# Kernel optimization log

Hardware: AMD Instinct MI355X
Metric: run time of the kernel (lower is better)

The kernel has to match this reference:

```python
import jax, jax.numpy as jnp
import numpy as np

SIGMA = 1.0


def setup_inputs() -> dict:
    key = jax.random.key(0)
    kx, kc = jax.random.split(key)
    B, C, H, W = 8, 64, 64, 64
    NUM_CENTERS = 16
    x = jax.random.normal(kx, (B, C, H, W), dtype=jnp.float32)
    centers = jax.random.normal(kc, (NUM_CENTERS,), dtype=jnp.float32)
    return {"x": x, "centers": centers}


def reference(x, centers):
    # x: (B, C, H, W), centers: (K,)
    B, C, H, W = x.shape
    xr = x.reshape(B, C, H * W, 1)                  # (B, C, HW, 1)
    dist_euc = jnp.abs(xr - centers)                # (B, C, HW, K)
    # soft assignment: softmax over centers of -sigma * |x - c|
    phi_soft = jax.nn.softmax(-SIGMA * dist_euc, axis=-1)
    softout = jnp.sum(phi_soft * centers, axis=-1)  # (B, C, HW)
    # hard assignment: argmax of softmax(-1e7 * |x-c|^2) == nearest center
    idx = jnp.argmin(dist_euc * dist_euc, axis=-1)  # (B, C, HW)
    hardout = centers[idx]                          # (B, C, HW)
    # straight-through: forward = hard, gradient = soft path
    out = jax.lax.stop_gradient(hardout - softout) + softout
    return out.reshape(B, C, H, W)
```

## Files before the change

### kernel.cpp

```cpp
#include <hip/hip_runtime.h>

#define NUM_CENTERS 16

__device__ __forceinline__ float nearest_center(float v, const float* __restrict__ c) {
    float best_val = c[0];
    float best_d   = fabsf(v - c[0]);
#pragma unroll
    for (int i = 1; i < NUM_CENTERS; ++i) {
        float d = fabsf(v - c[i]);
        if (d < best_d) { best_d = d; best_val = c[i]; }
    }
    return best_val;
}

__global__ __launch_bounds__(256) void nearest_center_kernel(
    const float* __restrict__ x,
    const float* __restrict__ centers,
    float* __restrict__ out,
    int n4)
{
    float c[NUM_CENTERS];
#pragma unroll
    for (int i = 0; i < NUM_CENTERS; ++i) c[i] = centers[i];

    int idx = blockIdx.x * blockDim.x + threadIdx.x;
    if (idx < n4) {
        float4 v = reinterpret_cast<const float4*>(x)[idx];
        float4 r;
        r.x = nearest_center(v.x, c);
        r.y = nearest_center(v.y, c);
        r.z = nearest_center(v.z, c);
        r.w = nearest_center(v.w, c);
        reinterpret_cast<float4*>(out)[idx] = r;
    }
}

extern "C" void kernel_launch(void* const* d_in, const int* in_sizes, int n_in,
                              void* d_out, int out_size, void* d_ws, size_t ws_size,
                              hipStream_t stream) {
    const float* x       = (const float*)d_in[0];
    const float* centers = (const float*)d_in[1];
    float* out           = (float*)d_out;

    int n  = in_sizes[0];
    int n4 = n / 4;

    const int block = 256;
    int grid = (n4 + block - 1) / block;
    nearest_center_kernel<<<grid, block, 0, stream>>>(x, centers, out, n4);
}
```

Measured before the change: 62.76 us.

## Use tree-reduction argmin, two float4s per thread, and nontemporal stores

```diff
diff --git a/kernel.cpp b/kernel.cpp
--- a/kernel.cpp
+++ b/kernel.cpp
@@ -2,15 +2,35 @@
 
 #define NUM_CENTERS 16
 
+typedef float nfloat4 __attribute__((ext_vector_type(4)));
+
 __device__ __forceinline__ float nearest_center(float v, const float* __restrict__ c) {
-    float best_val = c[0];
-    float best_d   = fabsf(v - c[0]);
+    float d[NUM_CENTERS];
+    float val[NUM_CENTERS];
 #pragma unroll
-    for (int i = 1; i < NUM_CENTERS; ++i) {
-        float d = fabsf(v - c[i]);
-        if (d < best_d) { best_d = d; best_val = c[i]; }
+    for (int i = 0; i < NUM_CENTERS; ++i) {
+        d[i]   = fabsf(v - c[i]);
+        val[i] = c[i];
     }
-    return best_val;
+#pragma unroll
+    for (int stride = 1; stride < NUM_CENTERS; stride <<= 1) {
+#pragma unroll
+        for (int i = 0; i < NUM_CENTERS; i += 2 * stride) {
+            bool r = d[i + stride] < d[i];
+            d[i]   = r ? d[i + stride]   : d[i];
+            val[i] = r ? val[i + stride] : val[i];
+        }
+    }
+    return val[0];
+}
+
+__device__ __forceinline__ nfloat4 map4(nfloat4 v, const float* __restrict__ c) {
+    nfloat4 r;
+    r.x = nearest_center(v.x, c);
+    r.y = nearest_center(v.y, c);
+    r.z = nearest_center(v.z, c);
+    r.w = nearest_center(v.w, c);
+    return r;
 }
 
 __global__ __launch_bounds__(256) void nearest_center_kernel(
@@ -23,15 +43,29 @@
 #pragma unroll
     for (int i = 0; i < NUM_CENTERS; ++i) c[i] = centers[i];
 
-    int idx = blockIdx.x * blockDim.x + threadIdx.x;
-    if (idx < n4) {
-        float4 v = reinterpret_cast<const float4*>(x)[idx];
-        float4 r;
-        r.x = nearest_center(v.x, c);
-        r.y = nearest_center(v.y, c);
-        r.z = nearest_center(v.z, c);
-        r.w = nearest_center(v.w, c);
-        reinterpret_cast<float4*>(out)[idx] = r;
+    const nfloat4* __restrict__ xv = reinterpret_cast<const nfloat4*>(x);
+    nfloat4* __restrict__ ov       = reinterpret_cast<nfloat4*>(out);
+
+    int t        = blockIdx.x * blockDim.x + threadIdx.x;
+    int nthreads = gridDim.x * blockDim.x;
+
+    int i0 = t;
+    int i1 = t + nthreads;
+
+    bool p0 = i0 < n4;
+    bool p1 = i1 < n4;
+
+    nfloat4 v0, v1;
+    if (p0) v0 = xv[i0];
+    if (p1) v1 = xv[i1];
+
+    if (p0) {
+        nfloat4 r0 = map4(v0, c);
+        __builtin_nontemporal_store(r0, ov + i0);
+    }
+    if (p1) {
+        nfloat4 r1 = map4(v1, c);
+        __builtin_nontemporal_store(r1, ov + i1);
     }
 }
 
@@ -46,6 +80,8 @@
     int n4 = n / 4;
 
     const int block = 256;
-    int grid = (n4 + block - 1) / block;
+    const int f4_per_thread = 2;
+    int threads_needed = (n4 + f4_per_thread - 1) / f4_per_thread;
+    int grid = (threads_needed + block - 1) / block;
     nearest_center_kernel<<<grid, block, 0, stream>>>(x, centers, out, n4);
 }
```

New measurement: 84.66 us. 34.9% more time.
